# Optimization experiments

Measured on AMD Instinct MI355X. Metric: run time of the kernel, lower is better.

The kernel has to match this reference:

```python
import jax, jax.numpy as jnp
import numpy as np

EPS = 1e-5  # torch BatchNorm default eps


def bn_silu(h, g, b, m, v):
    # eval-mode BatchNorm followed by SiLU (spnn.BatchNorm + spnn.SiLU on node features)
    return jax.nn.silu((h - m) * jax.lax.rsqrt(v + EPS) * g + b)


def sparse_conv(h, idx, valid, W, bias):
    # submanifold sparse conv as gather + per-offset matmul + accumulate
    # h: [N, Ci], idx/valid: [K, N], W: [K, Ci, Co]
    g = h[idx] * valid[..., None].astype(h.dtype)  # [K, N, Ci]
    return jnp.einsum('knc,kcf->nf', g, W) + bias


def setup_inputs() -> dict:
    key = jax.random.key(0)
    ks = jax.random.split(key, 16)
    N, C, B, NE, K = 100000, 64, 16, 256, 27
    x = jax.random.normal(ks[0], (N, C), jnp.float32)
    t = jax.random.normal(ks[1], (B, NE), jnp.float32)
    b = jnp.sort(jax.random.randint(ks[2], (N,), 0, B)).astype(jnp.int32)
    kmap_idx = jax.random.randint(ks[3], (K, N), 0, N).astype(jnp.int32)
    kmap_valid = (jax.random.uniform(ks[4], (K, N)) < 0.5).astype(jnp.int32)
    # center offset is the node itself and always present
    kmap_idx = kmap_idx.at[K // 2].set(jnp.arange(N, dtype=jnp.int32))
    kmap_valid = kmap_valid.at[K // 2].set(1)

    def nrm(k, shape, s=1.0):
        return jax.random.normal(k, shape, jnp.float32) * s

    return {
        'x': x, 't': t, 'b': b, 'kmap_idx': kmap_idx, 'kmap_valid': kmap_valid,
        'bn1_g': 1.0 + nrm(ks[5], (C,), 0.1), 'bn1_b': nrm(ks[6], (C,), 0.1),
        'bn1_m': nrm(ks[7], (C,), 0.1), 'bn1_v': jax.random.uniform(ks[8], (C,)) + 0.5,
        'W1': nrm(ks[9], (K, C, C), 0.02), 'b1c': nrm(ks[10], (C,), 0.02),
        'bn2_g': 1.0 + nrm(ks[11], (C,), 0.1), 'bn2_b': nrm(ks[12], (C,), 0.1),
        'bn2_m': nrm(ks[13], (C,), 0.1), 'bn2_v': jax.random.uniform(ks[14], (C,)) + 0.5,
        'W2': nrm(ks[15], (K, C, C), 0.02), 'b2c': nrm(jax.random.fold_in(key, 100), (C,), 0.02),
        'Wt': nrm(jax.random.fold_in(key, 101), (NE, 2 * C), 0.05),
        'bt': nrm(jax.random.fold_in(key, 102), (2 * C,), 0.02),
    }


def reference(x, t, b, kmap_idx, kmap_valid,
              bn1_g, bn1_b, bn1_m, bn1_v, W1, b1c,
              bn2_g, bn2_b, bn2_m, bn2_v, W2, b2c,
              Wt, bt):
    # conv1 = BN -> SiLU -> sparse Conv3d
    h = sparse_conv(bn_silu(x, bn1_g, bn1_b, bn1_m, bn1_v), kmap_idx, kmap_valid, W1, b1c)
    # TimeEmbeddingBlock: per-batch FiLM, gathered per node via batch index b
    tp = jax.nn.silu(t) @ Wt + bt              # [B, 2*nf]
    scale, shift = jnp.split(tp, 2, axis=-1)   # [B, nf] each
    h = (1.0 + scale[b]) * h + shift[b]
    # conv2 = BN -> SiLU -> sparse Conv3d
    h = sparse_conv(bn_silu(h, bn2_g, bn2_b, bn2_m, bn2_v), kmap_idx, kmap_valid, W2, b2c)
    # residual; ni == nf so idconv is identity (fc.noop)
    return h + x
```

## Files before the change

### kernel.cpp

```cpp
#include <hip/hip_runtime.h>

typedef __attribute__((ext_vector_type(16))) float f32x16;
typedef __attribute__((ext_vector_type(2))) long lv2;
typedef __attribute__((ext_vector_type(2))) unsigned int uint2v;

#define BN_EPS 1e-5f
#define KOFF 27
#define LSTRIDE 72

static __device__ __forceinline__ float silu_f(float z) {
  return z / (1.f + __expf(-z));
}

static __device__ __forceinline__ unsigned char f2fp8(float v) {
  unsigned int p = (unsigned int)__builtin_amdgcn_cvt_pk_fp8_f32(v, 0.f, 0, 0);
  return (unsigned char)(p & 0xffu);
}

__global__ void prep_all(const float* __restrict__ t, const float* __restrict__ Wt,
                         const float* __restrict__ bt,
                         float* __restrict__ scale_eff, float* __restrict__ shift,
                         const float* __restrict__ W1, const float* __restrict__ W2,
                         unsigned char* __restrict__ Wp1, unsigned char* __restrict__ Wp2,
                         const float* __restrict__ x, const float* __restrict__ g1,
                         const float* __restrict__ b1, const float* __restrict__ m1,
                         const float* __restrict__ v1, unsigned char* __restrict__ a1,
                         int total) {
  const int bid = blockIdx.x;
  if (bid < 864) {
    int tid = bid * 256 + threadIdx.x;
    const int tot = KOFF * 8 * 64 * 8;
    const float* W = W1;
    unsigned char* Wp = Wp1;
    if (tid >= tot) { tid -= tot; W = W2; Wp = Wp2; }
    int j = tid & 7, lane = (tid >> 3) & 63, f = (tid >> 9) & 7, k = tid >> 12;
    int ci = (f >> 1) * 16 + (lane >> 5) * 8 + j;
    int co = (f & 1) * 32 + (lane & 31);
    Wp[tid] = f2fp8(W[(k * 64 + ci) * 64 + co]);
  } else if (bid < 872) {
    int tid = (bid - 864) * 256 + threadIdx.x;
    int bi = tid >> 7, co = tid & 127;
    float acc = bt[co];
    for (int e = 0; e < 256; ++e) {
      float tv = t[bi * 256 + e];
      acc += silu_f(tv) * Wt[e * 128 + co];
    }
    if (co < 64) scale_eff[bi * 64 + co] = 1.f + acc;
    else         shift[bi * 64 + (co - 64)] = acc;
  } else {
    int i = ((bid - 872) * 256 + threadIdx.x) * 8;
    if (i >= total) {
      if (i < total + 64) *(uint2v*)(a1 + i) = (uint2v){0u, 0u};
      return;
    }
    float4 va = *(const float4*)(x + i);
    float4 vb = *(const float4*)(x + i + 4);
    int c = i & 63;
    float4 ga = *(const float4*)(g1 + c), gb = *(const float4*)(g1 + c + 4);
    float4 ba = *(const float4*)(b1 + c), bbv = *(const float4*)(b1 + c + 4);
    float4 ma = *(const float4*)(m1 + c), mb = *(const float4*)(m1 + c + 4);
    float4 vva = *(const float4*)(v1 + c), vvb = *(const float4*)(v1 + c + 4);
    float z0 = silu_f((va.x - ma.x) * (ga.x * rsqrtf(vva.x + BN_EPS)) + ba.x);
    float z1 = silu_f((va.y - ma.y) * (ga.y * rsqrtf(vva.y + BN_EPS)) + ba.y);
    float z2 = silu_f((va.z - ma.z) * (ga.z * rsqrtf(vva.z + BN_EPS)) + ba.z);
    float z3 = silu_f((va.w - ma.w) * (ga.w * rsqrtf(vva.w + BN_EPS)) + ba.w);
    float z4 = silu_f((vb.x - mb.x) * (gb.x * rsqrtf(vvb.x + BN_EPS)) + bbv.x);
    float z5 = silu_f((vb.y - mb.y) * (gb.y * rsqrtf(vvb.y + BN_EPS)) + bbv.y);
    float z6 = silu_f((vb.z - mb.z) * (gb.z * rsqrtf(vvb.z + BN_EPS)) + bbv.z);
    float z7 = silu_f((vb.w - mb.w) * (gb.w * rsqrtf(vvb.w + BN_EPS)) + bbv.w);
    unsigned int w0 = (unsigned int)__builtin_amdgcn_cvt_pk_fp8_f32(z0, z1, 0, 0);
    w0 = (unsigned int)__builtin_amdgcn_cvt_pk_fp8_f32(z2, z3, (int)w0, 1);
    unsigned int w1 = (unsigned int)__builtin_amdgcn_cvt_pk_fp8_f32(z4, z5, 0, 0);
    w1 = (unsigned int)__builtin_amdgcn_cvt_pk_fp8_f32(z6, z7, (int)w1, 1);
    *(uint2v*)(a1 + i) = (uint2v){w0, w1};
  }
}

template <int MODE>
__global__ __launch_bounds__(256, 6) void conv_k(
    const unsigned char* __restrict__ act, const int* __restrict__ idx,
    const int* __restrict__ valid, int* __restrict__ rowse,
    const unsigned char* __restrict__ Wp,
    const float* __restrict__ bias,
    const float* __restrict__ scale_eff, const float* __restrict__ shift,
    const int* __restrict__ bidx,
    const float* __restrict__ g2, const float* __restrict__ b2,
    const float* __restrict__ m2, const float* __restrict__ v2,
    const float* __restrict__ xres,
    unsigned char* __restrict__ out8, float* __restrict__ out_f, int N) {
  __shared__ unsigned char ldsA[2][64 * LSTRIDE];
  __shared__ unsigned char ldsW[2][4096];

  if (MODE == 0 && blockIdx.x == 0 && threadIdx.x < 64) {
    out8[(size_t)N * 64 + threadIdx.x] = 0;
  }
  const int tid = threadIdx.x;
  const int lane = tid & 63;
  const int wid = tid >> 6;
  const int half = lane >> 5;
  const int r32 = lane & 31;
  const int n0 = blockIdx.x * 64;

  const int q0 = lane & 3;
  const int rL = wid * 16 + (lane >> 2);
  const int nS = min(n0 + rL, N - 1);
  const int RH = wid >> 1;
  const int cb = wid & 1;

  f32x16 acc;
#pragma unroll
  for (int i = 0; i < 16; ++i) acc[i] = 0.f;

  int rvA, rvB;
  lv2 st0, st1, st2;
  lv2 wstA, wstB;

#define LDVG(kk) ({ \
    int _r; \
    if (MODE == 0) { \
      int _v = valid[(size_t)(kk) * N + nS]; \
      int _g = idx[(size_t)(kk) * N + nS]; \
      _r = _v ? _g : N; \
      if (q0 == 0) __builtin_nontemporal_store(_r, rowse + (size_t)(kk) * N + nS); \
    } else { \
      _r = rowse[(size_t)(kk) * N + nS]; \
    } \
    _r; })

#define GLOAD(st, rv) do { \
    st = *(const lv2*)(act + (size_t)(rv) * 64 + q0 * 16); \
  } while (0)

#define WGLOAD(kk, wst) do { \
    wst = *(const lv2*)(Wp + (size_t)(kk) * 4096 + tid * 16); \
  } while (0)

#define DSWRITE(buf, st) do { \
    unsigned char* _p = &ldsA[buf][rL * LSTRIDE + q0 * 16]; \
    *(long*)_p = st.x; \
    *(long*)(_p + 8) = st.y; \
  } while (0)

#define DSWRITE_W(buf, wst) do { \
    unsigned char* _p = &ldsW[buf][tid * 16]; \
    *(long*)_p = wst.x; \
    *(long*)(_p + 8) = wst.y; \
  } while (0)

#define COMPUTE(buf) do { \
    _Pragma("unroll") \
    for (int ks = 0; ks < 4; ++ks) { \
      long av = *(const long*)(&ldsA[buf][(RH * 32 + r32) * LSTRIDE + ks * 16 + half * 8]); \
      long wv = *(const long*)(&ldsW[buf][((ks * 2 + cb) * 64 + lane) * 8]); \
      acc = __builtin_amdgcn_mfma_f32_32x32x16_fp8_fp8(av, wv, acc, 0, 0, 0); \
    } } while (0)

#define BARRIER() do { \
    asm volatile("s_waitcnt lgkmcnt(0)" ::: "memory"); \
    __builtin_amdgcn_s_barrier(); \
  } while (0)

  rvA = LDVG(0);
  GLOAD(st0, rvA);
  rvB = LDVG(1);
  GLOAD(st1, rvB);
  rvA = LDVG(2);
  GLOAD(st2, rvA);
  rvB = LDVG(3);
  rvA = 0;
  WGLOAD(0, wstA);
  WGLOAD(1, wstB);
  DSWRITE(0, st0);
  DSWRITE_W(0, wstA);
  BARRIER();

#pragma unroll
  for (int k = 0; k < KOFF; ++k) {
    if (k + 1 < KOFF) {
      const int s = (k + 1) % 3;
      if (s == 0)      DSWRITE((k + 1) & 1, st0);
      else if (s == 1) DSWRITE((k + 1) & 1, st1);
      else             DSWRITE((k + 1) & 1, st2);
      if ((k + 1) & 1) DSWRITE_W(1, wstB); else DSWRITE_W(0, wstA);
    }
    if (k + 2 < KOFF) {
      if (k & 1) WGLOAD(k + 2, wstB); else WGLOAD(k + 2, wstA);
    }
    if (k + 3 < KOFF) {
      const int s = (k + 3) % 3;
      if ((k + 1) & 1) {
        if (s == 0) GLOAD(st0, rvB); else if (s == 1) GLOAD(st1, rvB); else GLOAD(st2, rvB);
      } else {
        if (s == 0) GLOAD(st0, rvA); else if (s == 1) GLOAD(st1, rvA); else GLOAD(st2, rvA);
      }
    }
    if (k + 4 < KOFF) {
      if (k & 1) rvB = LDVG(k + 4); else rvA = LDVG(k + 4);
    }
    COMPUTE(k & 1);
    if (k + 1 < KOFF) BARRIER();
  }
#undef LDVG
#undef GLOAD
#undef WGLOAD
#undef DSWRITE
#undef DSWRITE_W
#undef COMPUTE
#undef BARRIER

  if (MODE == 0) {
    const int c = cb * 32 + r32;
    float bb = bias[c];
    float s2v = g2[c] * rsqrtf(v2[c] + BN_EPS);
    float o2v = b2[c] - m2[c] * s2v;
#pragma unroll
    for (int r = 0; r < 16; ++r) {
      int rowD = (r & 3) + 8 * (r >> 2) + 4 * half;
      int n = n0 + RH * 32 + rowD;
      if (n < N) {
        int bi = bidx[n];
        float h = acc[r] + bb;
        h = scale_eff[bi * 64 + c] * h + shift[bi * 64 + c];
        float z = h * s2v + o2v;
        out8[(size_t)n * 64 + c] = f2fp8(silu_f(z));
      }
    }
  } else {
    const int c = cb * 32 + r32;
    float bb = bias[c];
#pragma unroll
    for (int r = 0; r < 16; ++r) {
      int rowD = (r & 3) + 8 * (r >> 2) + 4 * half;
      int n = n0 + RH * 32 + rowD;
      if (n < N) {
        out_f[(size_t)n * 64 + c] = acc[r] + bb + xres[(size_t)n * 64 + c];
      }
    }
  }
}

extern "C" void kernel_launch(void* const* d_in, const int* in_sizes, int n_in,
                              void* d_out, int out_size, void* d_ws, size_t ws_size,
                              hipStream_t stream) {
  const float* x    = (const float*)d_in[0];
  const float* t    = (const float*)d_in[1];
  const int*   b    = (const int*)d_in[2];
  const int*   kidx = (const int*)d_in[3];
  const int*   kval = (const int*)d_in[4];
  const float* bn1g = (const float*)d_in[5];
  const float* bn1b = (const float*)d_in[6];
  const float* bn1m = (const float*)d_in[7];
  const float* bn1v = (const float*)d_in[8];
  const float* W1   = (const float*)d_in[9];
  const float* b1c  = (const float*)d_in[10];
  const float* bn2g = (const float*)d_in[11];
  const float* bn2b = (const float*)d_in[12];
  const float* bn2m = (const float*)d_in[13];
  const float* bn2v = (const float*)d_in[14];
  const float* W2   = (const float*)d_in[15];
  const float* b2c  = (const float*)d_in[16];
  const float* Wt   = (const float*)d_in[17];
  const float* bt   = (const float*)d_in[18];
  float* out = (float*)d_out;

  const int N = in_sizes[2];
  const int total = N * 64;

  char* ws = (char*)d_ws;
  size_t actB = ((size_t)(N + 1) * 64 + 255) & ~(size_t)255;
  unsigned char* a1 = (unsigned char*)ws;
  unsigned char* a2 = (unsigned char*)(ws + actB);
  const size_t wpackB = (size_t)KOFF * 8 * 64 * 8;
  unsigned char* W1p = (unsigned char*)(ws + 2 * actB);
  unsigned char* W2p = (unsigned char*)(ws + 2 * actB + wpackB);
  float* scale_eff = (float*)(ws + 2 * actB + 2 * wpackB);
  float* shiftp    = scale_eff + 16 * 64;
  int*   rows_enc  = (int*)(ws + 2 * actB + 2 * wpackB + 8192);

  int bnblk = (total / 8 + 8 + 255) / 256;
  prep_all<<<872 + bnblk, 256, 0, stream>>>(t, Wt, bt, scale_eff, shiftp,
                                            W1, W2, W1p, W2p,
                                            x, bn1g, bn1b, bn1m, bn1v, a1, total);

  int nblk = (N + 63) / 64;
  conv_k<0><<<nblk, 256, 0, stream>>>(a1, kidx, kval, rows_enc, W1p, b1c, scale_eff,
                                      shiftp, b, bn2g, bn2b, bn2m, bn2v,
                                      nullptr, a2, nullptr, N);
  conv_k<1><<<nblk, 256, 0, stream>>>(a2, nullptr, nullptr, rows_enc, W2p, b2c, nullptr,
                                      nullptr, nullptr, nullptr, nullptr, nullptr,
                                      nullptr, x, nullptr, out, N);
}
```

Before: 112.9 us.

## Stage kernel-map idx/valid through an LDS ring instead of an encoded rows buffer

Drops the intermediate rows_enc buffer that conv1 wrote and conv2 read back. Both conv kernels now read idx and valid directly. Each of the four lanes per row loads a different word (idx or valid for one of two offsets), writes it into a 3-group shared-memory ring, and the row index is resolved from LDS just before the activation gather. This removes the redundant per-lane index loads and the global store/reload round trip. In exchange, conv2 now reads two int arrays instead of one, and the pipelined loop gains extra LDS traffic and barrier-dependent ring timing.

```diff
diff --git a/kernel.cpp b/kernel.cpp
--- a/kernel.cpp
+++ b/kernel.cpp
@@ -79,7 +79,7 @@
 template <int MODE>
 __global__ __launch_bounds__(256, 6) void conv_k(
     const unsigned char* __restrict__ act, const int* __restrict__ idx,
-    const int* __restrict__ valid, int* __restrict__ rowse,
+    const int* __restrict__ valid,
     const unsigned char* __restrict__ Wp,
     const float* __restrict__ bias,
     const float* __restrict__ scale_eff, const float* __restrict__ shift,
@@ -90,6 +90,8 @@
     unsigned char* __restrict__ out8, float* __restrict__ out_f, int N) {
   __shared__ unsigned char ldsA[2][64 * LSTRIDE];
   __shared__ unsigned char ldsW[2][4096];
+  __shared__ int rI[3][2][64];
+  __shared__ int rV[3][2][64];
 
   if (MODE == 0 && blockIdx.x == 0 && threadIdx.x < 64) {
     out8[(size_t)N * 64 + threadIdx.x] = 0;
@@ -111,21 +113,23 @@
 #pragma unroll
   for (int i = 0; i < 16; ++i) acc[i] = 0.f;
 
-  int rvA, rvB;
   lv2 st0, st1, st2;
   lv2 wstA, wstB;
-
-#define LDVG(kk) ({ \
-    int _r; \
-    if (MODE == 0) { \
-      int _v = valid[(size_t)(kk) * N + nS]; \
-      int _g = idx[(size_t)(kk) * N + nS]; \
-      _r = _v ? _g : N; \
-      if (q0 == 0) __builtin_nontemporal_store(_r, rowse + (size_t)(kk) * N + nS); \
-    } else { \
-      _r = rowse[(size_t)(kk) * N + nS]; \
-    } \
-    _r; })
+  int gr = 0;
+
+#define GRPLOAD(g) do { \
+    int tp = min(2 * (g) + (q0 >> 1), KOFF - 1); \
+    const int* bp = (q0 & 1) ? valid : idx; \
+    gr = bp[(size_t)tp * N + nS]; \
+  } while (0)
+
+#define RINGWRITE(g) do { \
+    int* p = (q0 & 1) ? &rV[(g) % 3][q0 >> 1][rL] : &rI[(g) % 3][q0 >> 1][rL]; \
+    *p = gr; \
+  } while (0)
+
+#define RINGREAD(t) \
+    (rV[((t) >> 1) % 3][(t) & 1][rL] ? rI[((t) >> 1) % 3][(t) & 1][rL] : N)
 
 #define GLOAD(st, rv) do { \
     st = *(const lv2*)(act + (size_t)(rv) * 64 + q0 * 16); \
@@ -160,14 +164,18 @@
     __builtin_amdgcn_s_barrier(); \
   } while (0)
 
-  rvA = LDVG(0);
-  GLOAD(st0, rvA);
-  rvB = LDVG(1);
-  GLOAD(st1, rvB);
-  rvA = LDVG(2);
-  GLOAD(st2, rvA);
-  rvB = LDVG(3);
-  rvA = 0;
+  GRPLOAD(0); RINGWRITE(0);
+  GRPLOAD(1); RINGWRITE(1);
+  GRPLOAD(2); RINGWRITE(2);
+  BARRIER();
+  {
+    int rv0 = RINGREAD(0);
+    GLOAD(st0, rv0);
+    int rv1 = RINGREAD(1);
+    GLOAD(st1, rv1);
+    int rv2 = RINGREAD(2);
+    GLOAD(st2, rv2);
+  }
   WGLOAD(0, wstA);
   WGLOAD(1, wstB);
   DSWRITE(0, st0);
@@ -183,24 +191,24 @@
       else             DSWRITE((k + 1) & 1, st2);
       if ((k + 1) & 1) DSWRITE_W(1, wstB); else DSWRITE_W(0, wstA);
     }
+    if (!(k & 1) && k <= 20) GRPLOAD((k + 6) / 2);
+    if ((k & 1) && k <= 21)  RINGWRITE((k + 5) / 2);
     if (k + 2 < KOFF) {
       if (k & 1) WGLOAD(k + 2, wstB); else WGLOAD(k + 2, wstA);
     }
     if (k + 3 < KOFF) {
+      int rv = RINGREAD(k + 3);
       const int s = (k + 3) % 3;
-      if ((k + 1) & 1) {
-        if (s == 0) GLOAD(st0, rvB); else if (s == 1) GLOAD(st1, rvB); else GLOAD(st2, rvB);
-      } else {
-        if (s == 0) GLOAD(st0, rvA); else if (s == 1) GLOAD(st1, rvA); else GLOAD(st2, rvA);
-      }
-    }
-    if (k + 4 < KOFF) {
-      if (k & 1) rvB = LDVG(k + 4); else rvA = LDVG(k + 4);
+      if (s == 0)      GLOAD(st0, rv);
+      else if (s == 1) GLOAD(st1, rv);
+      else             GLOAD(st2, rv);
     }
     COMPUTE(k & 1);
     if (k + 1 < KOFF) BARRIER();
   }
-#undef LDVG
+#undef GRPLOAD
+#undef RINGWRITE
+#undef RINGREAD
 #undef GLOAD
 #undef WGLOAD
 #undef DSWRITE
@@ -275,7 +283,6 @@
   unsigned char* W2p = (unsigned char*)(ws + 2 * actB + wpackB);
   float* scale_eff = (float*)(ws + 2 * actB + 2 * wpackB);
   float* shiftp    = scale_eff + 16 * 64;
-  int*   rows_enc  = (int*)(ws + 2 * actB + 2 * wpackB + 8192);
 
   int bnblk = (total / 8 + 8 + 255) / 256;
   prep_all<<<872 + bnblk, 256, 0, stream>>>(t, Wt, bt, scale_eff, shiftp,
@@ -283,10 +290,10 @@
                                             x, bn1g, bn1b, bn1m, bn1v, a1, total);
 
   int nblk = (N + 63) / 64;
-  conv_k<0><<<nblk, 256, 0, stream>>>(a1, kidx, kval, rows_enc, W1p, b1c, scale_eff,
+  conv_k<0><<<nblk, 256, 0, stream>>>(a1, kidx, kval, W1p, b1c, scale_eff,
                                       shiftp, b, bn2g, bn2b, bn2m, bn2v,
                                       nullptr, a2, nullptr, N);
-  conv_k<1><<<nblk, 256, 0, stream>>>(a2, nullptr, nullptr, rows_enc, W2p, b2c, nullptr,
+  conv_k<1><<<nblk, 256, 0, stream>>>(a2, kidx, kval, W2p, b2c, nullptr, nullptr,
                                       nullptr, nullptr, nullptr, nullptr, nullptr,
-                                      nullptr, x, nullptr, out, N);
-}
+                                      x, nullptr, out, N);
+}
```

Result: faster. 100.1 us (-11.3%).
